# Optimization experiments

Hardware: AMD Instinct MI355X
Metric: run time of the kernel (lower is better)

Reference implementation:

```python
import jax, jax.numpy as jnp
import numpy as np

B, N, C = 16, 4096, 80
IOU_THR = 0.5
CONF_THR = 0.5
MAX_DET = 100
FROM_LOGITS = True


def setup_inputs() -> dict:
    key = jax.random.key(0)
    k1, k2 = jax.random.split(key)
    box_prediction = jax.random.uniform(k1, (B, N, 4), dtype=jnp.float32)
    class_prediction = jax.random.normal(k2, (B, N, C), dtype=jnp.float32)
    return {"box_prediction": box_prediction, "class_prediction": class_prediction}


def _pairwise_iou(b):
    # TF NMS kernel semantics: corners [y1,x1,y2,x2], normalized with min/max.
    y1 = jnp.minimum(b[:, 0], b[:, 2]); y2 = jnp.maximum(b[:, 0], b[:, 2])
    x1 = jnp.minimum(b[:, 1], b[:, 3]); x2 = jnp.maximum(b[:, 1], b[:, 3])
    area = (y2 - y1) * (x2 - x1)                      # [N]
    ih = jnp.maximum(0.0, jnp.minimum(y2[:, None], y2[None, :]) - jnp.maximum(y1[:, None], y1[None, :]))
    iw = jnp.maximum(0.0, jnp.minimum(x2[:, None], x2[None, :]) - jnp.maximum(x1[:, None], x1[None, :]))
    inter = ih * iw                                   # [N, N]
    union = area[:, None] + area[None, :] - inter
    return jnp.where(inter > 0.0, inter / union, 0.0)


def _nms_single(boxes, cls):
    # boxes [N,4], cls [N,C] -> padded ([MAX_DET,4], [MAX_DET,C])
    scores = jnp.max(cls, axis=1)                     # tf.reduce_max(cls_pred, axis=1)
    order = jnp.argsort(-scores)                      # descending, stable
    b = boxes[order]
    s = scores[order]
    valid = s > CONF_THR                              # score_threshold filter
    iou = _pairwise_iou(b)                            # [N, N]

    def body(keep, i):
        suppressed = jnp.any(keep & (iou[:, i] > IOU_THR))
        k = valid[i] & jnp.logical_not(suppressed)
        return keep.at[i].set(k), None

    keep, _ = jax.lax.scan(body, jnp.zeros(boxes.shape[0], dtype=bool), jnp.arange(boxes.shape[0]))
    # Compact kept boxes to the front (stable sort keeps descending-score order),
    # take the first MAX_DET slots, zero-pad the rest (fixed-shape analogue of
    # tf.image.non_max_suppression's variable-length index output).
    pos = jnp.argsort(jnp.logical_not(keep))[:MAX_DET]
    m = (jnp.arange(MAX_DET) < jnp.sum(keep))[:, None]
    out_idx = order[pos]
    nms_box = jnp.where(m, boxes[out_idx], 0.0)
    nms_cls = jnp.where(m, cls[out_idx], 0.0)
    return nms_box, nms_cls


def reference(box_prediction, class_prediction):
    # bounding_box_format == 'xywh' (absolute) -> convert_format is identity.
    if FROM_LOGITS:
        cls_predictions = jax.nn.softmax(jnp.square(class_prediction * 10.0), axis=-1)
    else:
        cls_predictions = class_prediction
    nms_box, nms_cls = jax.vmap(_nms_single)(box_prediction, cls_predictions)
    return nms_box, nms_cls, cls_predictions
```

## Files before the change

kernel.cpp:

```cpp
#include <hip/hip_runtime.h>
#include <cstdint>
#include <cstddef>

#define BB 16
#define NN 4096
#define CC 80
#define MAXD 100
#define CONF_T 0.5f
#define RSTRIDE 81
#define PER_B (MAXD * 4 + MAXD * CC)
#define NWORDS 64
#define BCAP 4096
#define FBCAP 2048
#define SEGSZ 2048
#define CH 1024
#define CCAP 1088

#define IOUC 0x1.000001p-1

#define WS_KEYS   0x000000
#define WS_NLIST  0x1C0000
#define WS_KIDX   0x1C0100
#define WS_CNT    0x1C2000
#define WS_NEED   0x200000

__global__ __launch_bounds__(128) void k_softmax(const float* __restrict__ cls_in,
                                                 float* __restrict__ probs,
                                                 uint64_t* __restrict__ keys) {
#pragma clang fp contract(off)
    __shared__ float buf[128 * RSTRIDE];
    int t = threadIdx.x;
    size_t gbase = (size_t)blockIdx.x * 128 * CC;

    for (int i = t; i < 128 * CC; i += 128) {
        int r = i / CC, c = i - r * CC;
        buf[r * RSTRIDE + c] = cls_in[gbase + i];
    }
    __syncthreads();

    float* row = buf + t * RSTRIDE;

    float m = -3.402823466e+38f;
    for (int c = 0; c < CC; ++c) {
        float y = row[c] * 10.0f;
        float z = y * y;
        m = fmaxf(m, z);
    }
    for (int c = 0; c < CC; ++c) {
        float y = row[c] * 10.0f;
        float z = y * y;
        row[c] = expf(z - m);
    }
    float r8[8];
    #pragma unroll
    for (int j = 0; j < 8; ++j) r8[j] = row[j];
    for (int i = 8; i < CC; i += 8) {
        #pragma unroll
        for (int j = 0; j < 8; ++j) r8[j] += row[i + j];
    }
    float s = ((r8[0] + r8[1]) + (r8[2] + r8[3])) + ((r8[4] + r8[5]) + (r8[6] + r8[7]));

    float score = 1.0f / s;
    for (int c = 0; c < CC; ++c) row[c] = row[c] * score;

    int gw = blockIdx.x * 128 + t;
    unsigned n = (unsigned)(gw & (NN - 1));
    keys[gw] = ((uint64_t)__float_as_uint(score) << 32)
             | (uint64_t)(0xFFFFFFFFu - n);

    __syncthreads();
    for (int i = t; i < 128 * CC; i += 128) {
        int r = i / CC, c = i - r * CC;
        probs[gbase + i] = buf[r * RSTRIDE + c];
    }
}

__global__ __launch_bounds__(1024) void k_pnms(const uint64_t* __restrict__ keys,
                                               const float* __restrict__ boxes,
                                               int* __restrict__ kidx_out,
                                               int* __restrict__ cnt_out) {
#pragma clang fp contract(off)
    __shared__ __align__(16) unsigned char sraw[6 * NN * 4];
    float* hy1 = (float*)sraw;
    float* hx1 = (float*)(sraw + NN * 4);
    float* hy2 = (float*)(sraw + 2 * NN * 4);
    float* hx2 = (float*)(sraw + 3 * NN * 4);
    float* har = (float*)(sraw + 4 * NN * 4);
    int*   og  = (int*)(sraw + 5 * NN * 4);
    uint64_t* bbuf = (uint64_t*)sraw;
    __shared__ int clist[CCAP];
    __shared__ uint64_t kill[64];
    __shared__ int cand_s[64];
    __shared__ int kpos[MAXD];
    __shared__ int wsumA[16], wsumB[16], wsumC[16];
    __shared__ int kept_s, fk0_s, done_s, ccnt_s, cur_s;

    const int tid = threadIdx.x, lane = tid & 63, wv = tid >> 6;
    const int b = blockIdx.x;
    const uint64_t* kb = keys + (size_t)b * NN;
    const float* bxp = boxes + (size_t)b * NN * 4;

    uint64_t myk[4]; bool fa[4], fb[4];
    int asum = 0, bsum = 0;
    for (int k = 0; k < 4; ++k) {
        uint64_t key = kb[4 * tid + k]; myk[k] = key;
        unsigned hi = (unsigned)(key >> 32);
        fa[k] = (hi == 0x3F800000u);
        fb[k] = (__uint_as_float(hi) > CONF_T) && !fa[k];
        asum += fa[k] ? 1 : 0; bsum += fb[k] ? 1 : 0;
    }
    int ia = asum, ib = bsum;
    for (int off = 1; off < 64; off <<= 1) {
        int va = __shfl_up(ia, off), vb = __shfl_up(ib, off);
        if (lane >= off) { ia += va; ib += vb; }
    }
    if (lane == 63) { wsumA[wv] = ia; wsumB[wv] = ib; }
    __syncthreads();
    int baseA = 0, baseB = 0, cntA = 0, cntB = 0;
    for (int w2 = 0; w2 < 16; ++w2) {
        if (w2 < wv) { baseA += wsumA[w2]; baseB += wsumB[w2]; }
        cntA += wsumA[w2]; cntB += wsumB[w2];
    }
    int pA = baseA + (ia - asum);
    int pB = baseB + (ib - bsum);
    for (int k = 0; k < 4; ++k) {
        if (fa[k]) og[pA++] = 4 * tid + k;
        if (fb[k]) bbuf[pB++] = myk[k];
    }
    __syncthreads();

    for (int i = tid; i < cntB; i += 1024) {
        uint64_t ki = bbuf[i];
        int rank = 0;
        for (int j = 0; j < cntB; ++j) rank += (bbuf[j] > ki) ? 1 : 0;
        og[cntA + rank] = (int)(0xFFFFFFFFu - (unsigned)(ki & 0xFFFFFFFFull));
    }
    int nl = cntA + cntB; if (nl > NN) nl = NN;
    __syncthreads();

    for (int i = tid; i < nl; i += 1024) {
        int o = og[i];
        float4 bv = ((const float4*)bxp)[o];
        float y1 = fminf(bv.x, bv.z), y2 = fmaxf(bv.x, bv.z);
        float x1 = fminf(bv.y, bv.w), x2 = fmaxf(bv.y, bv.w);
        hy1[i] = y1; hx1[i] = x1; hy2[i] = y2; hx2[i] = x2;
        har[i] = (y2 - y1) * (x2 - x1);
    }
    if (tid == 0) { kept_s = 0; fk0_s = 0; done_s = 0; ccnt_s = 0; cur_s = 0; }

    for (;;) {
        __syncthreads();
        for (;;) {
            int cc0 = ccnt_s, cur = cur_s;
            if (cc0 >= 64 || cur >= nl) break;
            int i = cur + tid;
            bool v = i < nl;
            int ii = v ? i : 0;
            float y1 = hy1[ii], x1 = hx1[ii], y2 = hy2[ii], x2 = hx2[ii], ar = har[ii];
            bool sup = false;
            int f1 = kept_s;
            for (int q0 = 0; q0 < f1; q0 += 64) {
                int qi = q0 + lane;
                int kp = (qi < f1) ? kpos[qi] : 0;
                float ky1 = hy1[kp], kx1 = hx1[kp], ky2 = hy2[kp], kx2 = hx2[kp], kar = har[kp];
                int qn = f1 - q0; if (qn > 64) qn = 64;
                bool deadall = false;
                for (int q = 0; q < qn; ++q) {
                    float qy1 = __shfl(ky1, q), qx1 = __shfl(kx1, q);
                    float qy2 = __shfl(ky2, q), qx2 = __shfl(kx2, q);
                    float qar = __shfl(kar, q);
                    float ih = fmaxf(0.f, fminf(y2, qy2) - fmaxf(y1, qy1));
                    float iw = fmaxf(0.f, fminf(x2, qx2) - fmaxf(x1, qx1));
                    float inter = ih * iw;
                    float uni = (ar + qar) - inter;
                    sup = sup || (inter > 0.f && (double)inter > (double)uni * IOUC);
                    if ((q & 7) == 7 && __ballot(v && !sup) == 0ull) { deadall = true; break; }
                }
                if (deadall) break;
            }
            bool srv = v && !sup;
            int sflag = srv ? 1 : 0;
            int inc = sflag;
            for (int off = 1; off < 64; off <<= 1) {
                int v2 = __shfl_up(inc, off);
                if (lane >= off) inc += v2;
            }
            if (lane == 63) wsumC[wv] = inc;
            __syncthreads();
            int base = 0, tot = 0;
            for (int w2 = 0; w2 < 16; ++w2) {
                int s2 = wsumC[w2];
                if (w2 < wv) base += s2;
                tot += s2;
            }
            if (srv) clist[cc0 + base + (inc - sflag)] = i;
            if (tid == 0) { ccnt_s = cc0 + tot; cur_s = cur + CH; }
            __syncthreads();
        }
        int cc = ccnt_s;
        int st = cc < 64 ? cc : 64;
        if (tid < 64) cand_s[tid] = (tid < st) ? clist[tid] : -1;
        __syncthreads();
        if (st <= 0) break;

        {
            int cj = cand_s[lane];
            bool jv = cj >= 0;
            int cjx = jv ? cj : 0;
            float jy1 = hy1[cjx], jx1 = hx1[cjx], jy2 = hy2[cjx], jx2 = hx2[cjx], jar = har[cjx];
            #pragma unroll
            for (int r = 0; r < 4; ++r) {
                int t = wv + 16 * r;
                int ct = cand_s[t];
                bool tv = ct >= 0;
                int ctx = tv ? ct : 0;
                float ty1 = hy1[ctx], tx1 = hx1[ctx], ty2 = hy2[ctx], tx2 = hx2[ctx], tar = har[ctx];
                float ih = fmaxf(0.f, fminf(ty2, jy2) - fmaxf(ty1, jy1));
                float iw = fmaxf(0.f, fminf(tx2, jx2) - fmaxf(tx1, jx1));
                float inter = ih * iw;
                float uni = (tar + jar) - inter;
                bool s = tv && jv && (inter > 0.f) && ((double)inter > (double)uni * IOUC);
                uint64_t w = __ballot(s);
                if (lane == 0) kill[t] = w;
            }
        }
        __syncthreads();
        if (wv == 0) {
            uint64_t suppressed = 0, keptmask = 0;
            for (int j2 = 0; j2 < st; ++j2) {
                if (!((suppressed >> j2) & 1ull)) {
                    keptmask |= 1ull << j2;
                    suppressed |= kill[j2];
                }
            }
            int k0 = kept_s;
            if ((keptmask >> lane) & 1ull) {
                int pos = k0 + __popcll(keptmask & ((1ull << lane) - 1ull));
                if (pos < MAXD) kpos[pos] = cand_s[lane];
            }
            int k1 = k0 + __popcll(keptmask);
            if (lane == 0) {
                fk0_s = k0;
                kept_s = k1;
                done_s = (k1 >= MAXD || cc < 64) ? 1 : 0;
            }
        }
        __syncthreads();
        if (done_s) break;

        {
            int f0 = fk0_s, f1 = kept_s;
            int j = st + tid;
            bool v = j < cc;
            int idx = v ? clist[j] : 0;
            float y1 = hy1[idx], x1 = hx1[idx], y2 = hy2[idx], x2 = hx2[idx], ar = har[idx];
            bool sup = false;
            for (int q0 = f0; q0 < f1; q0 += 64) {
                int qi = q0 + lane;
                int kp = (qi < f1) ? kpos[qi] : 0;
                float ky1 = hy1[kp], kx1 = hx1[kp], ky2 = hy2[kp], kx2 = hx2[kp], kar = har[kp];
                int qn = f1 - q0; if (qn > 64) qn = 64;
                bool deadall = false;
                for (int q = 0; q < qn; ++q) {
                    float qy1 = __shfl(ky1, q), qx1 = __shfl(kx1, q);
                    float qy2 = __shfl(ky2, q), qx2 = __shfl(kx2, q);
                    float qar = __shfl(kar, q);
                    float ih = fmaxf(0.f, fminf(y2, qy2) - fmaxf(y1, qy1));
                    float iw = fmaxf(0.f, fminf(x2, qx2) - fmaxf(x1, qx1));
                    float inter = ih * iw;
                    float uni = (ar + qar) - inter;
                    sup = sup || (inter > 0.f && (double)inter > (double)uni * IOUC);
                    if ((q & 7) == 7 && __ballot(v && !sup) == 0ull) { deadall = true; break; }
                }
                if (deadall) break;
            }
            bool srv = v && !sup;
            int sflag = srv ? 1 : 0;
            int inc = sflag;
            for (int off = 1; off < 64; off <<= 1) {
                int v2 = __shfl_up(inc, off);
                if (lane >= off) inc += v2;
            }
            if (lane == 63) wsumC[wv] = inc;
            __syncthreads();
            int base = 0, tot = 0;
            for (int w2 = 0; w2 < 16; ++w2) {
                int s2 = wsumC[w2];
                if (w2 < wv) base += s2;
                tot += s2;
            }
            if (srv) clist[base + (inc - sflag)] = idx;
            if (tid == 0) ccnt_s = tot;
        }
    }

    int kt = kept_s; if (kt > MAXD) kt = MAXD;
    if (tid == 0) cnt_out[b] = kt;
    if (tid < MAXD) kidx_out[b * MAXD + tid] = (tid < kt) ? og[kpos[tid]] : 0;
}

__global__ __launch_bounds__(256) void k_gather(const float* __restrict__ boxes,
                                                const float* __restrict__ probs,
                                                const int* __restrict__ kidx,
                                                const int* __restrict__ cnt,
                                                float* __restrict__ out_box,
                                                float* __restrict__ out_cls) {
    int u = blockIdx.x * 256 + threadIdx.x;
    if (u >= BB * PER_B) return;
    int b = u / PER_B;
    int r = u - b * PER_B;
    int count = cnt[b];
    float val = 0.0f;
    if (r < MAXD * 4) {
        int t = r >> 2, e = r & 3;
        if (t < count) {
            int idx = kidx[b * MAXD + t];
            val = boxes[((size_t)b * NN + idx) * 4 + e];
        }
        out_box[(size_t)b * MAXD * 4 + r] = val;
    } else {
        int q = r - MAXD * 4;
        int t = q / CC, c = q - t * CC;
        if (t < count) {
            int idx = kidx[b * MAXD + t];
            val = probs[((size_t)b * NN + idx) * CC + c];
        }
        out_cls[(size_t)b * MAXD * CC + q] = val;
    }
}

__global__ __launch_bounds__(1024) void k_nms_fb(uint64_t* keys,
                                                 const float* __restrict__ boxes,
                                                 int* __restrict__ kidx_out,
                                                 int* __restrict__ cnt_out) {
#pragma clang fp contract(off)
    __shared__ float sy1[SEGSZ], sx1[SEGSZ], sy2[SEGSZ], sx2[SEGSZ];
    __shared__ int   soidx[SEGSZ];
    __shared__ uint64_t bbuf[FBCAP];
    __shared__ uint64_t sup[NWORDS];
    __shared__ float ky1[MAXD], kx1[MAXD], ky2[MAXD], kx2[MAXD], kar[MAXD];
    __shared__ int   keptidx[MAXD];
    __shared__ int   wsumA[16], wsumB[16];
    __shared__ int   keptcnt_s, ctrl_s, seg_s;

    const int tid = threadIdx.x, lane = tid & 63, wv = tid >> 6;
    const int b = blockIdx.x;
    const uint64_t* kb = keys + (size_t)b * NN;
    const float* bxp = boxes + (size_t)b * NN * 4;
    int* og = (int*)(keys + (size_t)b * NN);

    uint64_t myk[4]; bool fa[4], fb[4];
    int asum = 0, bsum = 0;
    for (int k = 0; k < 4; ++k) {
        uint64_t key = kb[4 * tid + k]; myk[k] = key;
        unsigned hi = (unsigned)(key >> 32);
        fa[k] = (hi == 0x3F800000u);
        fb[k] = (__uint_as_float(hi) > CONF_T) && !fa[k];
        asum += fa[k] ? 1 : 0; bsum += fb[k] ? 1 : 0;
    }
    int ia = asum, ib = bsum;
    for (int off = 1; off < 64; off <<= 1) {
        int va = __shfl_up(ia, off), vb = __shfl_up(ib, off);
        if (lane >= off) { ia += va; ib += vb; }
    }
    if (lane == 63) { wsumA[wv] = ia; wsumB[wv] = ib; }
    __syncthreads();
    int baseA = 0, baseB = 0, cntA = 0, cntB = 0;
    for (int w2 = 0; w2 < 16; ++w2) {
        if (w2 < wv) { baseA += wsumA[w2]; baseB += wsumB[w2]; }
        cntA += wsumA[w2]; cntB += wsumB[w2];
    }
    int pA = baseA + (ia - asum);
    int pB = baseB + (ib - bsum);
    for (int k = 0; k < 4; ++k) {
        if (fa[k]) og[pA++] = 4 * tid + k;
        if (fb[k]) { if (pB < FBCAP) bbuf[pB] = myk[k]; pB++; }
    }
    int cntBc = cntB < FBCAP ? cntB : FBCAP;
    int nlist = cntA + cntBc;
    if (tid == 0) { keptcnt_s = 0; seg_s = 0; }
    for (int i = tid; i < FBCAP; i += 1024) if (i >= cntB) bbuf[i] = 0;
    __syncthreads();

    for (unsigned k2 = 2; k2 <= FBCAP; k2 <<= 1) {
        for (unsigned j = k2 >> 1; j > 0; j >>= 1) {
            for (unsigned i = tid; i < FBCAP; i += 1024) {
                unsigned p = i ^ j;
                if (p > i) {
                    uint64_t va = bbuf[i], vb = bbuf[p];
                    bool desc = ((i & k2) == 0);
                    if (desc ? (va < vb) : (va > vb)) { bbuf[i] = vb; bbuf[p] = va; }
                }
            }
            __syncthreads();
        }
    }
    for (int i = tid; i < cntBc; i += 1024)
        og[cntA + i] = (int)(0xFFFFFFFFu - (unsigned)(bbuf[i] & 0xFFFFFFFFull));
    if (tid < NWORDS) {
        int lo = tid * 64;
        uint64_t mm;
        if (nlist <= lo) mm = ~0ull;
        else if (nlist >= lo + 64) mm = 0ull;
        else mm = (~0ull) << (nlist - lo);
        sup[tid] = mm;
    }
    __syncthreads();

    for (int i = tid; i < SEGSZ; i += 1024) {
        if (i < nlist) {
            int o = og[i];
            soidx[i] = o;
            const float* bp = bxp + (size_t)o * 4;
            float b0 = bp[0], b1 = bp[1], b2 = bp[2], b3 = bp[3];
            sy1[i] = fminf(b0, b2); sy2[i] = fmaxf(b0, b2);
            sx1[i] = fminf(b1, b3); sx2[i] = fmaxf(b1, b3);
        }
    }
    __syncthreads();

    int curw = 0, segr = 0;
    while (true) {
        if (tid == 0) {
            int code = -1;
            for (;;) {
                int wend = (segr + 1) * (SEGSZ / 64);
                if (curw >= wend) {
                    if (segr == 0 && nlist > SEGSZ) {
                        code = -2; segr = 1; seg_s = 1; curw = SEGSZ / 64;
                    } else code = -1;
                    break;
                }
                uint64_t live = ~sup[curw];
                if (live) {
                    int j = __ffsll((unsigned long long)live) - 1;
                    int sel = curw * 64 + j;
                    int li = sel - segr * SEGSZ;
                    int kc = keptcnt_s;
                    keptidx[kc] = soidx[li];
                    ky1[kc] = sy1[li]; kx1[kc] = sx1[li];
                    ky2[kc] = sy2[li]; kx2[kc] = sx2[li];
                    kar[kc] = (sy2[li] - sy1[li]) * (sx2[li] - sx1[li]);
                    keptcnt_s = kc + 1;
                    sup[curw] |= (1ull << j);
                    code = (kc + 1 >= MAXD) ? -1 : sel;
                    break;
                }
                ++curw;
            }
            ctrl_s = code;
        }
        __syncthreads();
        int c = ctrl_s;
        if (c == -1) break;

        if (c == -2) {
            for (int i = tid; i < SEGSZ; i += 1024) {
                int gi = SEGSZ + i;
                if (gi < nlist) {
                    int o = og[gi];
                    soidx[i] = o;
                    const float* bp = bxp + (size_t)o * 4;
                    float b0 = bp[0], b1 = bp[1], b2 = bp[2], b3 = bp[3];
                    sy1[i] = fminf(b0, b2); sy2[i] = fmaxf(b0, b2);
                    sx1[i] = fminf(b1, b3); sx2[i] = fmaxf(b1, b3);
                }
            }
            __syncthreads();
            int kc = keptcnt_s;
            for (int k = 0; k < 2; ++k) {
                int li = tid + k * 1024;
                float y1 = sy1[li], y2 = sy2[li], x1 = sx1[li], x2 = sx2[li];
                float ar = (y2 - y1) * (x2 - x1);
                bool s = false;
                for (int q = 0; q < kc; ++q) {
                    float ih = fmaxf(0.f, fminf(y2, ky2[q]) - fmaxf(y1, ky1[q]));
                    float iw = fmaxf(0.f, fminf(x2, kx2[q]) - fmaxf(x1, kx1[q]));
                    float inter = ih * iw;
                    float uni = (ar + kar[q]) - inter;
                    s = s || (inter > 0.f && inter / uni > 0.5f);
                }
                uint64_t bal = __ballot(s);
                if (lane == 0 && bal) {
                    int word = (SEGSZ + k * 1024 + wv * 64) >> 6;
                    sup[word] |= bal;
                }
            }
            __syncthreads();
            continue;
        }

        int sg = seg_s;
        int cl = c - sg * SEGSZ;
        float cy1 = sy1[cl], cy2 = sy2[cl], cx1 = sx1[cl], cx2 = sx2[cl];
        float car = (cy2 - cy1) * (cx2 - cx1);
        for (int k = 0; k < 2; ++k) {
            int li = tid + k * 1024;
            float y1 = sy1[li], y2 = sy2[li], x1 = sx1[li], x2 = sx2[li];
            float ar = (y2 - y1) * (x2 - x1);
            float ih = fmaxf(0.f, fminf(y2, cy2) - fmaxf(y1, cy1));
            float iw = fmaxf(0.f, fminf(x2, cx2) - fmaxf(x1, cx1));
            float inter = ih * iw;
            float uni = (ar + car) - inter;
            bool s = (inter > 0.f) && (inter / uni > 0.5f);
            uint64_t bal = __ballot(s);
            if (lane == 0 && bal) {
                int word = (sg * SEGSZ + k * 1024 + wv * 64) >> 6;
                sup[word] |= bal;
            }
        }
        __syncthreads();
    }

    if (tid == 0) cnt_out[b] = keptcnt_s;
    for (int i = tid; i < MAXD; i += 1024)
        kidx_out[b * MAXD + i] = (i < keptcnt_s) ? keptidx[i] : 0;
}

extern "C" void kernel_launch(void* const* d_in, const int* in_sizes, int n_in,
                              void* d_out, int out_size, void* d_ws, size_t ws_size,
                              hipStream_t stream) {
    const float* boxes = (const float*)d_in[0];
    const float* cls   = (const float*)d_in[1];
    float* out = (float*)d_out;
    float* out_box = out;
    float* out_cls = out + (size_t)BB * MAXD * 4;
    float* probs   = out + (size_t)BB * MAXD * 4 + (size_t)BB * MAXD * CC;

    char* ws = (char*)d_ws;
    uint64_t* keys = (uint64_t*)(ws + WS_KEYS);

    k_softmax<<<(BB * NN) / 128, 128, 0, stream>>>(cls, probs, keys);

    if (ws_size >= (size_t)WS_NEED) {
        int* kidx  = (int*)(ws + WS_KIDX);
        int* cnt   = (int*)(ws + WS_CNT);

        k_pnms<<<BB, 1024, 0, stream>>>(keys, boxes, kidx, cnt);
        k_gather<<<(BB * PER_B + 255) / 256, 256, 0, stream>>>(boxes, probs, kidx, cnt,
                                                               out_box, out_cls);
    } else {
        int* kidx = (int*)(ws + (size_t)BB * NN * sizeof(uint64_t));
        int* cnt  = kidx + BB * MAXD;
        k_nms_fb<<<BB, 1024, 0, stream>>>(keys, boxes, kidx, cnt);
        k_gather<<<(BB * PER_B + 255) / 256, 256, 0, stream>>>(boxes, probs, kidx, cnt,
                                                               out_box, out_cls);
    }
}
```

Before: 124.0 us.

## Parallelize softmax across 8 lanes per row and fuse gather into NMS kernel

Result: faster. 116.4 us (-6.1%).

```diff
diff --git a/kernel.cpp b/kernel.cpp
--- a/kernel.cpp
+++ b/kernel.cpp
@@ -7,10 +7,8 @@
 #define CC 80
 #define MAXD 100
 #define CONF_T 0.5f
-#define RSTRIDE 81
 #define PER_B (MAXD * 4 + MAXD * CC)
 #define NWORDS 64
-#define BCAP 4096
 #define FBCAP 2048
 #define SEGSZ 2048
 #define CH 1024
@@ -19,66 +17,57 @@
 #define IOUC 0x1.000001p-1
 
 #define WS_KEYS   0x000000
-#define WS_NLIST  0x1C0000
-#define WS_KIDX   0x1C0100
-#define WS_CNT    0x1C2000
 #define WS_NEED   0x200000
 
-__global__ __launch_bounds__(128) void k_softmax(const float* __restrict__ cls_in,
+__global__ __launch_bounds__(256) void k_softmax(const float* __restrict__ cls_in,
                                                  float* __restrict__ probs,
                                                  uint64_t* __restrict__ keys) {
 #pragma clang fp contract(off)
-    __shared__ float buf[128 * RSTRIDE];
-    int t = threadIdx.x;
-    size_t gbase = (size_t)blockIdx.x * 128 * CC;
-
-    for (int i = t; i < 128 * CC; i += 128) {
-        int r = i / CC, c = i - r * CC;
-        buf[r * RSTRIDE + c] = cls_in[gbase + i];
-    }
-    __syncthreads();
-
-    float* row = buf + t * RSTRIDE;
-
+    int slot = blockIdx.x * 256 + threadIdx.x;
+    int row  = slot >> 3;
+    int j    = slot & 7;
+    const float* rp = cls_in + (size_t)row * CC + j;
+
+    float e[10];
     float m = -3.402823466e+38f;
-    for (int c = 0; c < CC; ++c) {
-        float y = row[c] * 10.0f;
+    #pragma unroll
+    for (int k = 0; k < 10; ++k) {
+        float y = rp[8 * k] * 10.0f;
         float z = y * y;
+        e[k] = z;
         m = fmaxf(m, z);
     }
-    for (int c = 0; c < CC; ++c) {
-        float y = row[c] * 10.0f;
-        float z = y * y;
-        row[c] = expf(z - m);
-    }
-    float r8[8];
+    m = fmaxf(m, __shfl_xor(m, 1));
+    m = fmaxf(m, __shfl_xor(m, 2));
+    m = fmaxf(m, __shfl_xor(m, 4));
+
     #pragma unroll
-    for (int j = 0; j < 8; ++j) r8[j] = row[j];
-    for (int i = 8; i < CC; i += 8) {
-        #pragma unroll
-        for (int j = 0; j < 8; ++j) r8[j] += row[i + j];
-    }
-    float s = ((r8[0] + r8[1]) + (r8[2] + r8[3])) + ((r8[4] + r8[5]) + (r8[6] + r8[7]));
-
-    float score = 1.0f / s;
-    for (int c = 0; c < CC; ++c) row[c] = row[c] * score;
-
-    int gw = blockIdx.x * 128 + t;
-    unsigned n = (unsigned)(gw & (NN - 1));
-    keys[gw] = ((uint64_t)__float_as_uint(score) << 32)
-             | (uint64_t)(0xFFFFFFFFu - n);
-
-    __syncthreads();
-    for (int i = t; i < 128 * CC; i += 128) {
-        int r = i / CC, c = i - r * CC;
-        probs[gbase + i] = buf[r * RSTRIDE + c];
+    for (int k = 0; k < 10; ++k) e[k] = expf(e[k] - m);
+
+    float acc = e[0];
+    #pragma unroll
+    for (int k = 1; k < 10; ++k) acc += e[k];
+    acc = acc + __shfl_xor(acc, 1);
+    acc = acc + __shfl_xor(acc, 2);
+    acc = acc + __shfl_xor(acc, 4);
+
+    float score = 1.0f / acc;
+    float* pp = probs + (size_t)row * CC + j;
+    #pragma unroll
+    for (int k = 0; k < 10; ++k) pp[8 * k] = e[k] * score;
+
+    if (j == 0) {
+        unsigned n = (unsigned)(row & (NN - 1));
+        keys[row] = ((uint64_t)__float_as_uint(score) << 32)
+                  | (uint64_t)(0xFFFFFFFFu - n);
     }
 }
 
 __global__ __launch_bounds__(1024) void k_pnms(const uint64_t* __restrict__ keys,
                                                const float* __restrict__ boxes,
-                                               int* __restrict__ kidx_out,
-                                               int* __restrict__ cnt_out) {
+                                               const float* __restrict__ probs,
+                                               float* __restrict__ out_box,
+                                               float* __restrict__ out_cls) {
 #pragma clang fp contract(off)
     __shared__ __align__(16) unsigned char sraw[6 * NN * 4];
     float* hy1 = (float*)sraw;
@@ -295,8 +284,24 @@
     }
 
     int kt = kept_s; if (kt > MAXD) kt = MAXD;
-    if (tid == 0) cnt_out[b] = kt;
-    if (tid < MAXD) kidx_out[b * MAXD + tid] = (tid < kt) ? og[kpos[tid]] : 0;
+    if (tid < MAXD) clist[tid] = (tid < kt) ? og[kpos[tid]] : 0;
+    __syncthreads();
+
+    float* ob = out_box + (size_t)b * MAXD * 4;
+    float* oc = out_cls + (size_t)b * MAXD * CC;
+    const float* pb = probs + (size_t)b * NN * CC;
+    for (int r = tid; r < MAXD * 4; r += 1024) {
+        int t = r >> 2, e2 = r & 3;
+        float val = 0.0f;
+        if (t < kt) { int idx = clist[t]; val = bxp[(size_t)idx * 4 + e2]; }
+        ob[r] = val;
+    }
+    for (int q = tid; q < MAXD * CC; q += 1024) {
+        int t = q / CC, c = q - t * CC;
+        float val = 0.0f;
+        if (t < kt) { int idx = clist[t]; val = pb[(size_t)idx * CC + c]; }
+        oc[q] = val;
+    }
 }
 
 __global__ __launch_bounds__(256) void k_gather(const float* __restrict__ boxes,
@@ -530,15 +535,10 @@
     char* ws = (char*)d_ws;
     uint64_t* keys = (uint64_t*)(ws + WS_KEYS);
 
-    k_softmax<<<(BB * NN) / 128, 128, 0, stream>>>(cls, probs, keys);
+    k_softmax<<<(BB * NN * 8) / 256, 256, 0, stream>>>(cls, probs, keys);
 
     if (ws_size >= (size_t)WS_NEED) {
-        int* kidx  = (int*)(ws + WS_KIDX);
-        int* cnt   = (int*)(ws + WS_CNT);
-
-        k_pnms<<<BB, 1024, 0, stream>>>(keys, boxes, kidx, cnt);
-        k_gather<<<(BB * PER_B + 255) / 256, 256, 0, stream>>>(boxes, probs, kidx, cnt,
-                                                               out_box, out_cls);
+        k_pnms<<<BB, 1024, 0, stream>>>(keys, boxes, probs, out_box, out_cls);
     } else {
         int* kidx = (int*)(ws + (size_t)BB * NN * sizeof(uint64_t));
         int* cnt  = kidx + BB * MAXD;
```
